# Kernel optimization log

Measured on AMD Instinct MI355X. Metric: run time of the kernel, lower is better.

Reference implementation:

```python
import jax, jax.numpy as jnp
import numpy as np

B, S, D = 4, 2048, 1024
NEG = -1e10

def setup_inputs() -> dict:
    key = jax.random.key(0)
    ks = jax.random.split(key, 10)
    inv = 1.0 / np.sqrt(D)
    return {
        "Q": jax.random.normal(ks[0], (B, S, D), dtype=jnp.float32),
        "K": jax.random.normal(ks[1], (B, S, D), dtype=jnp.float32),
        "V": jax.random.normal(ks[2], (B, S, D), dtype=jnp.float32),
        "attention_mask": jax.random.randint(ks[3], (B, 1, S), 0, 2, dtype=jnp.int32),
        "Wq": jax.random.uniform(ks[4], (D, D), jnp.float32, -inv, inv),
        "bq": jnp.zeros((D,), jnp.float32),
        "Wk": jax.random.uniform(ks[5], (D, D), jnp.float32, -inv, inv),
        "bk": jnp.zeros((D,), jnp.float32),
        "Wv": jax.random.uniform(ks[6], (D, D), jnp.float32, -inv, inv),
        "bv": jnp.zeros((D,), jnp.float32),
    }

def reference(Q, K, V, attention_mask, Wq, bq, Wk, bk, Wv, bv):
    # QKV projections (dropout is identity in eval mode)
    q = jnp.einsum('bsd,ed->bse', Q, Wq) + bq  # [B,S,D]
    k = jnp.einsum('bsd,ed->bse', K, Wk) + bk
    v = jnp.einsum('bsd,ed->bse', V, Wv) + bv
    scores = jnp.einsum('bqd,bkd->bqk', q, k) / jnp.sqrt(jnp.float32(D))  # [B,S,S]
    scores = jnp.where(attention_mask == 0, jnp.float32(NEG), scores)
    # additive causal mask: upper triangle (diag=1) gets NEG
    causal = jnp.triu(jnp.full((S, S), NEG, dtype=jnp.float32), k=1)
    scores = scores + causal
    attn = jax.nn.softmax(scores, axis=-1)
    return jnp.einsum('bqk,bkd->bqd', attn, v)
```

## Files before the change

kernel.cpp:

```cpp
#include <hip/hip_runtime.h>
#include <hip/hip_bf16.h>

typedef __bf16 bf16x8 __attribute__((ext_vector_type(8)));
typedef float floatx4 __attribute__((ext_vector_type(4)));
typedef unsigned short ushort_t;

__device__ __forceinline__ bf16x8 load8f(const float* p) {
  const float4* q = reinterpret_cast<const float4*>(p);
  float4 x = q[0], y = q[1];
  bf16x8 r;
  r[0] = (__bf16)x.x; r[1] = (__bf16)x.y; r[2] = (__bf16)x.z; r[3] = (__bf16)x.w;
  r[4] = (__bf16)y.x; r[5] = (__bf16)y.y; r[6] = (__bf16)y.z; r[7] = (__bf16)y.w;
  return r;
}

__device__ __forceinline__ void storeC(float* C, long idx, float v) { C[idx] = v; }
__device__ __forceinline__ void storeC(ushort_t* C, long idx, float v) {
  __bf16 b = (__bf16)v;
  C[idx] = __builtin_bit_cast(ushort_t, b);
}

__device__ __forceinline__ void glds16(const ushort_t* g, ushort_t* l) {
  __builtin_amdgcn_global_load_lds(
      (const __attribute__((address_space(1))) void*)g,
      (__attribute__((address_space(3))) void*)l, 16, 0, 0);
}

__device__ __forceinline__ void bar_raw()  { asm volatile("s_barrier" ::: "memory"); }
__device__ __forceinline__ void wait_vm0() { asm volatile("s_waitcnt vmcnt(0)" ::: "memory"); }
__device__ __forceinline__ void wlg12() {
  asm volatile("s_waitcnt lgkmcnt(12)" ::: "memory");
  __builtin_amdgcn_sched_barrier(0);
}
__device__ __forceinline__ void wlg8() {
  asm volatile("s_waitcnt lgkmcnt(8)" ::: "memory");
  __builtin_amdgcn_sched_barrier(0);
}
__device__ __forceinline__ void wlg0() {
  asm volatile("s_waitcnt lgkmcnt(0)" ::: "memory");
  __builtin_amdgcn_sched_barrier(0);
}

__global__ __launch_bounds__(256) void cvt3m(
    const float* __restrict__ Q, const float* __restrict__ K,
    const float* __restrict__ V, const float* __restrict__ Wq,
    const float* __restrict__ Wk, const float* __restrict__ Wv,
    ushort_t* __restrict__ dstQ, ushort_t* __restrict__ dstW,
    long nq, long nw,
    const int* __restrict__ mask, int* __restrict__ j0, int S, int B)
{
  const int z = blockIdx.y;
  const long bq = nq >> 11;
  long x = blockIdx.x;
  const float* s; ushort_t* d; long n;
  if (x < bq) {
    s = (z == 0) ? Q : ((z == 1) ? K : V);
    d = dstQ + (long)z * nq; n = nq;
  } else {
    x -= bq;
    s = (z == 0) ? Wq : ((z == 1) ? Wk : Wv);
    d = dstW + (long)z * nw; n = nw;
  }
  const long i = ((x * 256) + threadIdx.x) * 8;
  if (i < n) {
    bf16x8 v = load8f(s + i);
    *reinterpret_cast<bf16x8*>(d + i) = v;
  }
  if (z == 0 && (int)blockIdx.x < B) {
    const int b = blockIdx.x;
    const int* m = mask + (long)b * S;
    const int tid = threadIdx.x;
    int best = S;
    for (int j = tid; j < S; j += 256)
      if (m[j] != 0) best = min(best, j);
    #pragma unroll
    for (int off = 32; off; off >>= 1)
      best = min(best, __shfl_xor(best, off));
    __shared__ int red[4];
    if ((tid & 63) == 0) red[tid >> 6] = best;
    __syncthreads();
    if (tid == 0) j0[b] = min(min(red[0], red[1]), min(red[2], red[3]));
  }
}

template<typename TC>
__device__ __forceinline__ void gemm256_core(
    const ushort_t* __restrict__ Apan,
    const ushort_t* __restrict__ Bpan,
    const float* __restrict__ bias, int bias_mode,
    TC* __restrict__ C, int bm, int bn, int N, int K, int G, float alpha)
{
  __shared__ ushort_t Ab[2][2][128 * 64];
  __shared__ ushort_t Bb[2][2][128 * 64];

  const int tid = threadIdx.x;
  const int wv = tid >> 6;
  const int lane = tid & 63;
  const int wr = wv >> 2, wc = wv & 3;
  const int lr = lane & 15, lq = lane >> 4;

  const int q0 = tid << 4;
  const int r0 = q0 >> 7;
  const int c0 = ((q0 & 127) ^ ((r0 & 7) << 4)) >> 1;
  const int lo0 = q0 >> 1;
  const int lo1 = lo0 + 4096;
  const long Kl = K;

  const ushort_t* As0 = Apan + (long)r0 * Kl + c0;
  const ushort_t* Bs0 = Bpan + (long)r0 * Kl + c0;

  auto stA = [&](int t, int h) {
    const ushort_t* s = As0 + (long)(h * 128) * Kl + t * 64;
    ushort_t* d = &Ab[t & 1][h][0];
    glds16(s, d + lo0);
    glds16(s + 64 * Kl, d + lo1);
  };
  auto stB = [&](int t, int h) {
    const ushort_t* s = Bs0 + (long)(h * 128) * Kl + t * 64;
    ushort_t* d = &Bb[t & 1][h][0];
    glds16(s, d + lo0);
    glds16(s + 64 * Kl, d + lo1);
  };

  const int aco0 = ((lq * 16) ^ ((lr & 7) << 4)) >> 1;
  const int aco1 = ((64 + lq * 16) ^ ((lr & 7) << 4)) >> 1;

  floatx4 acc[8][4];
  #pragma unroll
  for (int i = 0; i < 8; ++i)
    #pragma unroll
    for (int j = 0; j < 4; ++j)
      acc[i][j] = (floatx4){0.f, 0.f, 0.f, 0.f};

  bf16x8 a0[4][2], a1[4][2], b0[2][2], b1[2][2];

  auto ldA4 = [&](bf16x8 (&a)[4][2], int buf, int i0) {
    const ushort_t* Ah = &Ab[buf][wr][lr * 64];
    #pragma unroll
    for (int i = 0; i < 4; ++i) {
      a[i][0] = *reinterpret_cast<const bf16x8*>(Ah + (i0 + i) * 1024 + aco0);
      a[i][1] = *reinterpret_cast<const bf16x8*>(Ah + (i0 + i) * 1024 + aco1);
    }
  };
  auto ldB2 = [&](bf16x8 (&b)[2][2], int buf, int j0) {
    const ushort_t* Bh = &Bb[buf][wc >> 1][(wc & 1) * 4096 + lr * 64];
    #pragma unroll
    for (int j = 0; j < 2; ++j) {
      b[j][0] = *reinterpret_cast<const bf16x8*>(Bh + (j0 + j) * 1024 + aco0);
      b[j][1] = *reinterpret_cast<const bf16x8*>(Bh + (j0 + j) * 1024 + aco1);
    }
  };
  auto MM = [&](int I0, bf16x8 (&AF)[4][2], int J0, bf16x8 (&BF)[2][2]) {
    #pragma unroll
    for (int i = 0; i < 4; ++i)
      #pragma unroll
      for (int j = 0; j < 2; ++j) {
        acc[I0 + i][J0 + j] = __builtin_amdgcn_mfma_f32_16x16x32_bf16(
            AF[i][0], BF[j][0], acc[I0 + i][J0 + j], 0, 0, 0);
        acc[I0 + i][J0 + j] = __builtin_amdgcn_mfma_f32_16x16x32_bf16(
            AF[i][1], BF[j][1], acc[I0 + i][J0 + j], 0, 0, 0);
      }
  };

  stA(0, 0); stA(0, 1); stB(0, 0); stB(0, 1);
  wait_vm0();
  bar_raw();

  for (int t = 0; t < G; ++t) {
    const int buf = t & 1;
    if (t + 1 < G) { stA(t + 1, 0); stA(t + 1, 1); stB(t + 1, 0); stB(t + 1, 1); }
    __builtin_amdgcn_sched_barrier(0);
    ldA4(a0, buf, 0);
    ldB2(b0, buf, 0);
    __builtin_amdgcn_sched_barrier(0);
    ldB2(b1, buf, 2);
    __builtin_amdgcn_sched_barrier(0);
    ldA4(a1, buf, 4);
    __builtin_amdgcn_sched_barrier(0);
    wlg12();
    __builtin_amdgcn_s_setprio(1);
    MM(0, a0, 0, b0);
    __builtin_amdgcn_s_setprio(0);
    wlg8();
    __builtin_amdgcn_s_setprio(1);
    MM(0, a0, 2, b1);
    __builtin_amdgcn_s_setprio(0);
    wlg0();
    __builtin_amdgcn_s_setprio(1);
    MM(4, a1, 0, b0);
    MM(4, a1, 2, b1);
    __builtin_amdgcn_s_setprio(0);
    wait_vm0();
    bar_raw();
  }

  #pragma unroll
  for (int i = 0; i < 8; ++i) {
    #pragma unroll
    for (int j = 0; j < 4; ++j) {
      const int row0 = bm * 256 + wr * 128 + i * 16 + lq * 4;
      const int col  = bn * 256 + wc * 64 + j * 16 + lr;
      #pragma unroll
      for (int r = 0; r < 4; ++r) {
        float v = acc[i][j][r] * alpha;
        if (bias_mode == 1) v += bias[col];
        else if (bias_mode == 2) v += bias[row0 + r];
        storeC(C, (long)(row0 + r) * N + col, v);
      }
    }
  }
}

__global__ __launch_bounds__(512) void proj8(
    const ushort_t* __restrict__ Qb, const ushort_t* __restrict__ Wqb,
    const float* __restrict__ bq, const float* __restrict__ bk,
    const float* __restrict__ bv,
    ushort_t* __restrict__ qk, ushort_t* __restrict__ vT,
    long NQ, long NW)
{
  const int h = blockIdx.x;
  const int s = (h & 7) * 48 + (h >> 3);
  int bm, bn, N, mode;
  const ushort_t *A, *Bp;
  ushort_t* Cc;
  const float* bias;
  if (s < 256) {
    const int z = s >> 7, r = s & 127;
    bm = r >> 2; bn = r & 3;
    A  = Qb + (long)z * NQ + (long)bm * 256 * 1024;
    Bp = Wqb + (long)z * NW + (long)bn * 256 * 1024;
    Cc = qk + (long)z * NQ;
    bias = z ? bk : bq; mode = 1; N = 1024;
  } else {
    const int u = s - 256, vb = u >> 5, r = u & 31;
    bm = r >> 3; bn = r & 7;
    A  = Wqb + 2 * NW + (long)bm * 256 * 1024;
    Bp = Qb + 2 * NQ + (long)vb * (2048L * 1024) + (long)bn * 256 * 1024;
    Cc = vT + (long)vb * (1024L * 2048);
    bias = bv; mode = 2; N = 2048;
  }
  gemm256_core<ushort_t>(A, Bp, bias, mode, Cc, bm, bn, N, 1024, 16, 1.0f);
}

__global__ __launch_bounds__(512) void scores8(
    const ushort_t* __restrict__ qb, const ushort_t* __restrict__ kb,
    ushort_t* __restrict__ Sc, const int* __restrict__ j0p)
{
  const int h = blockIdx.x;
  const int job = (h & 7) * 32 + (h >> 3);
  const int bz = job >> 6;
  const int s = job & 63;
  int bm, bn;
  if (s < 36) {
    int r = 0;
    while ((r + 1) * (r + 2) / 2 <= s) ++r;
    bm = r; bn = s - r * (r + 1) / 2;
  } else {
    int u = s - 36, r = 0;
    while (u >= 7 - r) { u -= 7 - r; ++r; }
    bm = r; bn = r + 1 + u;
  }
  if (bn > bm && j0p[bz] <= bm * 256) return;
  const long SD = 2048L * 1024;
  gemm256_core<ushort_t>(qb + (long)bz * SD + (long)bm * 256 * 1024,
                         kb + (long)bz * SD + (long)bn * 256 * 1024,
                         nullptr, 0, Sc + (long)bz * 2048 * 2048,
                         bm, bn, 2048, 1024, 16, 0.03125f);
}

__global__ __launch_bounds__(512) void pv8(
    const ushort_t* __restrict__ P, const ushort_t* __restrict__ vT,
    float* __restrict__ out, float* __restrict__ scr,
    const int* __restrict__ j0p)
{
  const int h = blockIdx.x;
  const int job = (h & 7) * 32 + (h >> 3);
  const int bz = job >> 6;
  const int r = job & 63;
  const int bm = r >> 3;
  const int kh = (r >> 2) & 1;
  const int bn = r & 3;

  const int Gf = (j0p[bz] <= bm * 256) ? (bm + 1) * 4 : 32;
  int g0, g1;
  if (Gf > 8) {
    const int half = Gf >> 1;
    g0 = kh ? half : 0;
    g1 = kh ? Gf : half;
  } else {
    if (kh) return;
    g0 = 0; g1 = Gf;
  }

  float* Cc = kh ? (scr + (long)bz * (2048L * 1024))
                 : (out + (long)bz * (2048L * 1024));
  gemm256_core<float>(
      P  + (long)bz * (2048L * 2048) + (long)bm * 256 * 2048 + g0 * 64,
      vT + (long)bz * (1024L * 2048) + (long)bn * 256 * 2048 + g0 * 64,
      nullptr, 0, Cc, bm, bn, 1024, 2048, g1 - g0, 1.0f);
}

__global__ __launch_bounds__(256) void pv_combine(
    float* __restrict__ out, const float* __restrict__ scr,
    const int* __restrict__ j0p)
{
  const long u = (((long)blockIdx.x * 256) + threadIdx.x) * 8;
  const int bz = (int)(u >> 21);
  const long rem = u & ((1L << 21) - 1);
  const int row = (int)(rem >> 10);
  const int bm = row >> 8;
  const int Gf = (j0p[bz] <= bm * 256) ? (bm + 1) * 4 : 32;
  if (Gf <= 8) return;
  float4* o = reinterpret_cast<float4*>(out + u);
  const float4* s = reinterpret_cast<const float4*>(scr + u);
  float4 o0 = o[0], o1 = o[1], s0 = s[0], s1 = s[1];
  o0.x += s0.x; o0.y += s0.y; o0.z += s0.z; o0.w += s0.w;
  o1.x += s1.x; o1.y += s1.y; o1.z += s1.z; o1.w += s1.w;
  o[0] = o0; o[1] = o1;
}

__global__ __launch_bounds__(256) void softmax_causal(
    const ushort_t* __restrict__ Sc, ushort_t* __restrict__ P,
    const int* __restrict__ mask, const int* __restrict__ j0p, int S)
{
  const int i = blockIdx.x, b = blockIdx.y;
  const ushort_t* row = Sc + ((long)b * S + i) * S;
  ushort_t* prow = P + ((long)b * S + i) * S;
  const int* mrow = mask + (long)b * S;
  const int tid = threadIdx.x;
  const int lane = tid & 63, wave = tid >> 6;
  const int j0 = tid * 8;
  __shared__ float red[4];

  const int blk = i >> 8;
  const int jmax = (j0p[b] <= (blk << 8)) ? ((blk + 1) << 8) : S;
  const bool act = (j0 < jmax);

  float vals[8];
  float mymax = -3.4e38f;
  if (act) {
    bf16x8 sv = *reinterpret_cast<const bf16x8*>(row + j0);
    const int4* mp = reinterpret_cast<const int4*>(mrow + j0);
    int4 m0 = mp[0], m1 = mp[1];
    int mk[8] = {m0.x, m0.y, m0.z, m0.w, m1.x, m1.y, m1.z, m1.w};
    #pragma unroll
    for (int u = 0; u < 8; ++u) {
      const int j = j0 + u;
      float v = (float)sv[u];
      if (mk[u] == 0) v = -1e10f;
      if (j > i) v += -1e10f;
      vals[u] = v;
      mymax = fmaxf(mymax, v);
    }
  }
  #pragma unroll
  for (int off = 32; off; off >>= 1)
    mymax = fmaxf(mymax, __shfl_xor(mymax, off));
  if (lane == 0) red[wave] = mymax;
  __syncthreads();
  const float m = fmaxf(fmaxf(red[0], red[1]), fmaxf(red[2], red[3]));
  __syncthreads();

  float sum = 0.f;
  if (act) {
    #pragma unroll
    for (int u = 0; u < 8; ++u) {
      const float e = __expf(vals[u] - m);
      vals[u] = e;
      sum += e;
    }
  }
  #pragma unroll
  for (int off = 32; off; off >>= 1)
    sum += __shfl_xor(sum, off);
  if (lane == 0) red[wave] = sum;
  __syncthreads();
  const float tot = red[0] + red[1] + red[2] + red[3];
  const float inv = 1.0f / tot;

  if (act) {
    bf16x8 pv;
    #pragma unroll
    for (int u = 0; u < 8; ++u) pv[u] = (__bf16)(vals[u] * inv);
    *reinterpret_cast<bf16x8*>(prow + j0) = pv;
  }
}

extern "C" void kernel_launch(void* const* d_in, const int* in_sizes, int n_in,
                              void* d_out, int out_size, void* d_ws, size_t ws_size,
                              hipStream_t stream)
{
  const int B = 4, S = 2048, D = 1024;
  const float* Q  = (const float*)d_in[0];
  const float* K  = (const float*)d_in[1];
  const float* V  = (const float*)d_in[2];
  const int*   am = (const int*)d_in[3];
  const float* Wq = (const float*)d_in[4];
  const float* bq = (const float*)d_in[5];
  const float* Wk = (const float*)d_in[6];
  const float* bk = (const float*)d_in[7];
  const float* Wv = (const float*)d_in[8];
  const float* bv = (const float*)d_in[9];
  float* out = (float*)d_out;

  const long MS = (long)B * S;
  const long NQ = MS * D;
  const long NW = (long)D * D;

  ushort_t* qb = (ushort_t*)d_ws;
  ushort_t* kb = qb + NQ;
  ushort_t* vT = kb + NQ;
  ushort_t* Qb = vT + NQ;
  ushort_t* Wqb = Qb + 3 * NQ;
  int* j0 = (int*)(Wqb + 3 * NW);
  ushort_t* Sc = Qb;
  ushort_t* P  = qb;
  float* scr   = (float*)Qb;

  cvt3m<<<dim3((int)(NQ / 2048 + NW / 2048), 3), dim3(256), 0, stream>>>(
      Q, K, V, Wq, Wk, Wv, Qb, Wqb, NQ, NW, am, j0, S, B);

  proj8<<<dim3(384), dim3(512), 0, stream>>>(Qb, Wqb, bq, bk, bv, qb, vT, NQ, NW);

  scores8<<<dim3(256), dim3(512), 0, stream>>>(qb, kb, Sc, j0);

  softmax_causal<<<dim3(S, B), dim3(256), 0, stream>>>(Sc, P, am, j0, S);

  pv8<<<dim3(256), dim3(512), 0, stream>>>(P, vT, out, scr, j0);
  pv_combine<<<dim3((int)(MS * D / 8 / 256)), dim3(256), 0, stream>>>(out, scr, j0);
}
```

Baseline: 325.3 us.

## Fuse fp32-to-bf16 activation conversion into projection GEMM loads

The separate pre-pass that converted the Q, K and V activations from fp32 to bf16 is removed. The projection GEMM now loads fp32 activation tiles into registers, packs them to bf16 and writes them to swizzled LDS, interleaved with the MFMA pipeline, while the weights keep the async global-to-LDS path. This removes a full read and write of the activation tensors through HBM. In exchange each GEMM reads twice as many bytes for activations and spends extra VGPRs and VALU work on conversion, which may cut latency hiding.

```diff
diff --git a/kernel.cpp b/kernel.cpp
--- a/kernel.cpp
+++ b/kernel.cpp
@@ -13,6 +13,12 @@
   r[4] = (__bf16)y.x; r[5] = (__bf16)y.y; r[6] = (__bf16)y.z; r[7] = (__bf16)y.w;
   return r;
 }
+__device__ __forceinline__ bf16x8 pack8(float4 x, float4 y) {
+  bf16x8 r;
+  r[0] = (__bf16)x.x; r[1] = (__bf16)x.y; r[2] = (__bf16)x.z; r[3] = (__bf16)x.w;
+  r[4] = (__bf16)y.x; r[5] = (__bf16)y.y; r[6] = (__bf16)y.z; r[7] = (__bf16)y.w;
+  return r;
+}
 
 __device__ __forceinline__ void storeC(float* C, long idx, float v) { C[idx] = v; }
 __device__ __forceinline__ void storeC(ushort_t* C, long idx, float v) {
@@ -28,6 +34,14 @@
 
 __device__ __forceinline__ void bar_raw()  { asm volatile("s_barrier" ::: "memory"); }
 __device__ __forceinline__ void wait_vm0() { asm volatile("s_waitcnt vmcnt(0)" ::: "memory"); }
+__device__ __forceinline__ void wv4s() {
+  asm volatile("s_waitcnt vmcnt(4)" ::: "memory");
+  __builtin_amdgcn_sched_barrier(0);
+}
+__device__ __forceinline__ void wv0s() {
+  asm volatile("s_waitcnt vmcnt(0)" ::: "memory");
+  __builtin_amdgcn_sched_barrier(0);
+}
 __device__ __forceinline__ void wlg12() {
   asm volatile("s_waitcnt lgkmcnt(12)" ::: "memory");
   __builtin_amdgcn_sched_barrier(0);
@@ -36,33 +50,25 @@
   asm volatile("s_waitcnt lgkmcnt(8)" ::: "memory");
   __builtin_amdgcn_sched_barrier(0);
 }
+__device__ __forceinline__ void wlg4() {
+  asm volatile("s_waitcnt lgkmcnt(4)" ::: "memory");
+  __builtin_amdgcn_sched_barrier(0);
+}
 __device__ __forceinline__ void wlg0() {
   asm volatile("s_waitcnt lgkmcnt(0)" ::: "memory");
   __builtin_amdgcn_sched_barrier(0);
 }
 
 __global__ __launch_bounds__(256) void cvt3m(
-    const float* __restrict__ Q, const float* __restrict__ K,
-    const float* __restrict__ V, const float* __restrict__ Wq,
-    const float* __restrict__ Wk, const float* __restrict__ Wv,
-    ushort_t* __restrict__ dstQ, ushort_t* __restrict__ dstW,
-    long nq, long nw,
+    const float* __restrict__ Wq, const float* __restrict__ Wk,
+    const float* __restrict__ Wv, ushort_t* __restrict__ dstW, long nw,
     const int* __restrict__ mask, int* __restrict__ j0, int S, int B)
 {
   const int z = blockIdx.y;
-  const long bq = nq >> 11;
-  long x = blockIdx.x;
-  const float* s; ushort_t* d; long n;
-  if (x < bq) {
-    s = (z == 0) ? Q : ((z == 1) ? K : V);
-    d = dstQ + (long)z * nq; n = nq;
-  } else {
-    x -= bq;
-    s = (z == 0) ? Wq : ((z == 1) ? Wk : Wv);
-    d = dstW + (long)z * nw; n = nw;
-  }
-  const long i = ((x * 256) + threadIdx.x) * 8;
-  if (i < n) {
+  const float* s = (z == 0) ? Wq : ((z == 1) ? Wk : Wv);
+  ushort_t* d = dstW + (long)z * nw;
+  const long i = (((long)blockIdx.x * 256) + threadIdx.x) * 8;
+  if (i < nw) {
     bf16x8 v = load8f(s + i);
     *reinterpret_cast<bf16x8*>(d + i) = v;
   }
@@ -85,8 +91,7 @@
 
 template<typename TC>
 __device__ __forceinline__ void gemm256_core(
-    const ushort_t* __restrict__ Apan,
-    const ushort_t* __restrict__ Bpan,
+    const ushort_t* __restrict__ Apan, const ushort_t* __restrict__ Bpan,
     const float* __restrict__ bias, int bias_mode,
     TC* __restrict__ C, int bm, int bn, int N, int K, int G, float alpha)
 {
@@ -211,35 +216,206 @@
   }
 }
 
-__global__ __launch_bounds__(512) void proj8(
-    const ushort_t* __restrict__ Qb, const ushort_t* __restrict__ Wqb,
+template<typename TC, bool F32A>
+__device__ __forceinline__ void gemm256f(
+    ushort_t* __restrict__ AbL, ushort_t* __restrict__ BbL,
+    const float* __restrict__ Fsrc, const ushort_t* __restrict__ Hsrc,
+    const float* __restrict__ bias, int bias_mode,
+    TC* __restrict__ C, int bm, int bn, int N, float alpha)
+{
+  const int K = 1024, G = 16;
+
+  const int tid = threadIdx.x;
+  const int wv = tid >> 6;
+  const int lane = tid & 63;
+  const int wr = wv >> 2, wc = wv & 3;
+  const int lr = lane & 15, lq = lane >> 4;
+
+  auto AB = [&](int buf, int h) -> ushort_t* { return AbL + ((buf * 2 + h) << 13); };
+  auto BB = [&](int buf, int h) -> ushort_t* { return BbL + ((buf * 2 + h) << 13); };
+
+  const int q0 = tid << 4;
+  const int r0 = q0 >> 7;
+  const int c0 = ((q0 & 127) ^ ((r0 & 7) << 4)) >> 1;
+  const int lo0 = q0 >> 1;
+  const int lo1 = lo0 + 4096;
+  const ushort_t* Hs0 = Hsrc + (long)r0 * K + c0;
+  auto stH = [&](int t) {
+    #pragma unroll
+    for (int h = 0; h < 2; ++h) {
+      const ushort_t* s = Hs0 + (long)(h * 128) * K + t * 64;
+      ushort_t* d = F32A ? BB(t & 1, h) : AB(t & 1, h);
+      glds16(s, d + lo0);
+      glds16(s + 64 * K, d + lo1);
+    }
+  };
+
+  const int rr = tid >> 1, cc = (tid & 1) << 5;
+  const int rl = rr & 127, hh = rr >> 7;
+  const int sw = (rl & 7) << 3;
+  const float* Fs0 = Fsrc + (long)rr * K + cc;
+  float4 fl0[4], fl1[4];
+  auto ldF0 = [&](int t) {
+    const float4* p = reinterpret_cast<const float4*>(Fs0 + t * 64);
+    #pragma unroll
+    for (int i = 0; i < 4; ++i) fl0[i] = p[i];
+  };
+  auto ldF1 = [&](int t) {
+    const float4* p = reinterpret_cast<const float4*>(Fs0 + t * 64 + 16);
+    #pragma unroll
+    for (int i = 0; i < 4; ++i) fl1[i] = p[i];
+  };
+  auto wrF0 = [&](int t) {
+    ushort_t* dst = (F32A ? AB(t & 1, hh) : BB(t & 1, hh)) + rl * 64;
+    *reinterpret_cast<bf16x8*>(dst + ((cc + 0) ^ sw)) = pack8(fl0[0], fl0[1]);
+    *reinterpret_cast<bf16x8*>(dst + ((cc + 8) ^ sw)) = pack8(fl0[2], fl0[3]);
+  };
+  auto wrF1 = [&](int t) {
+    ushort_t* dst = (F32A ? AB(t & 1, hh) : BB(t & 1, hh)) + rl * 64;
+    *reinterpret_cast<bf16x8*>(dst + ((cc + 16) ^ sw)) = pack8(fl1[0], fl1[1]);
+    *reinterpret_cast<bf16x8*>(dst + ((cc + 24) ^ sw)) = pack8(fl1[2], fl1[3]);
+  };
+
+  const int aco0 = ((lq * 16) ^ ((lr & 7) << 4)) >> 1;
+  const int aco1 = ((64 + lq * 16) ^ ((lr & 7) << 4)) >> 1;
+
+  floatx4 acc[8][4];
+  #pragma unroll
+  for (int i = 0; i < 8; ++i)
+    #pragma unroll
+    for (int j = 0; j < 4; ++j)
+      acc[i][j] = (floatx4){0.f, 0.f, 0.f, 0.f};
+
+  bf16x8 a0[4][2], a1[4][2], b0[2][2], b1[2][2];
+
+  auto ldA4 = [&](bf16x8 (&a)[4][2], int buf, int i0) {
+    const ushort_t* Ah = AB(buf, wr) + lr * 64;
+    #pragma unroll
+    for (int i = 0; i < 4; ++i) {
+      a[i][0] = *reinterpret_cast<const bf16x8*>(Ah + (i0 + i) * 1024 + aco0);
+      a[i][1] = *reinterpret_cast<const bf16x8*>(Ah + (i0 + i) * 1024 + aco1);
+    }
+  };
+  auto ldB2 = [&](bf16x8 (&b)[2][2], int buf, int j0) {
+    const ushort_t* Bh = BB(buf, wc >> 1) + (wc & 1) * 4096 + lr * 64;
+    #pragma unroll
+    for (int j = 0; j < 2; ++j) {
+      b[j][0] = *reinterpret_cast<const bf16x8*>(Bh + (j0 + j) * 1024 + aco0);
+      b[j][1] = *reinterpret_cast<const bf16x8*>(Bh + (j0 + j) * 1024 + aco1);
+    }
+  };
+  auto MM = [&](int I0, bf16x8 (&AF)[4][2], int J0, bf16x8 (&BF)[2][2]) {
+    #pragma unroll
+    for (int i = 0; i < 4; ++i)
+      #pragma unroll
+      for (int j = 0; j < 2; ++j) {
+        acc[I0 + i][J0 + j] = __builtin_amdgcn_mfma_f32_16x16x32_bf16(
+            AF[i][0], BF[j][0], acc[I0 + i][J0 + j], 0, 0, 0);
+        acc[I0 + i][J0 + j] = __builtin_amdgcn_mfma_f32_16x16x32_bf16(
+            AF[i][1], BF[j][1], acc[I0 + i][J0 + j], 0, 0, 0);
+      }
+  };
+
+  ldF0(0); stH(0);
+  wv4s();
+  wrF0(0);
+  ldF1(0);
+  wv0s();
+  wrF1(0);
+  wlg0();
+  bar_raw();
+
+  for (int t = 0; t < G; ++t) {
+    const int buf = t & 1;
+    const bool pre = (t + 1 < G);
+    if (pre) {
+      ldF0(t + 1);
+      stH(t + 1);
+    }
+    __builtin_amdgcn_sched_barrier(0);
+    ldA4(a0, buf, 0);
+    ldB2(b0, buf, 0);
+    __builtin_amdgcn_sched_barrier(0);
+    ldB2(b1, buf, 2);
+    __builtin_amdgcn_sched_barrier(0);
+    wlg4();
+    __builtin_amdgcn_s_setprio(1);
+    MM(0, a0, 0, b0);
+    __builtin_amdgcn_s_setprio(0);
+    wlg0();
+    __builtin_amdgcn_s_setprio(1);
+    MM(0, a0, 2, b1);
+    __builtin_amdgcn_s_setprio(0);
+    if (pre) {
+      wv4s();
+      wrF0(t + 1);
+      ldF1(t + 1);
+      __builtin_amdgcn_sched_barrier(0);
+    }
+    ldA4(a1, buf, 4);
+    __builtin_amdgcn_sched_barrier(0);
+    wlg0();
+    __builtin_amdgcn_s_setprio(1);
+    MM(4, a1, 0, b0);
+    MM(4, a1, 2, b1);
+    __builtin_amdgcn_s_setprio(0);
+    if (pre) {
+      wv0s();
+      wrF1(t + 1);
+      wlg0();
+    } else {
+      wait_vm0();
+    }
+    bar_raw();
+  }
+
+  #pragma unroll
+  for (int i = 0; i < 8; ++i) {
+    #pragma unroll
+    for (int j = 0; j < 4; ++j) {
+      const int row0 = bm * 256 + wr * 128 + i * 16 + lq * 4;
+      const int col  = bn * 256 + wc * 64 + j * 16 + lr;
+      #pragma unroll
+      for (int r = 0; r < 4; ++r) {
+        float v = acc[i][j][r] * alpha;
+        if (bias_mode == 1) v += bias[col];
+        else if (bias_mode == 2) v += bias[row0 + r];
+        storeC(C, (long)(row0 + r) * N + col, v);
+      }
+    }
+  }
+}
+
+__global__ __launch_bounds__(512) void projF(
+    const float* __restrict__ Qf, const float* __restrict__ Kf,
+    const float* __restrict__ Vf, const ushort_t* __restrict__ Wb,
     const float* __restrict__ bq, const float* __restrict__ bk,
     const float* __restrict__ bv,
     ushort_t* __restrict__ qk, ushort_t* __restrict__ vT,
     long NQ, long NW)
 {
+  __shared__ ushort_t AbS[2][2][128 * 64];
+  __shared__ ushort_t BbS[2][2][128 * 64];
+  ushort_t* AbL = &AbS[0][0][0];
+  ushort_t* BbL = &BbS[0][0][0];
+
   const int h = blockIdx.x;
   const int s = (h & 7) * 48 + (h >> 3);
-  int bm, bn, N, mode;
-  const ushort_t *A, *Bp;
-  ushort_t* Cc;
-  const float* bias;
   if (s < 256) {
     const int z = s >> 7, r = s & 127;
-    bm = r >> 2; bn = r & 3;
-    A  = Qb + (long)z * NQ + (long)bm * 256 * 1024;
-    Bp = Wqb + (long)z * NW + (long)bn * 256 * 1024;
-    Cc = qk + (long)z * NQ;
-    bias = z ? bk : bq; mode = 1; N = 1024;
+    const int bm = r >> 2, bn = r & 3;
+    const float* F = (z ? Kf : Qf) + (long)bm * 256 * 1024;
+    const ushort_t* H = Wb + (long)z * NW + (long)bn * 256 * 1024;
+    gemm256f<ushort_t, true>(AbL, BbL, F, H, z ? bk : bq, 1,
+                             qk + (long)z * NQ, bm, bn, 1024, 1.0f);
   } else {
     const int u = s - 256, vb = u >> 5, r = u & 31;
-    bm = r >> 3; bn = r & 7;
-    A  = Wqb + 2 * NW + (long)bm * 256 * 1024;
-    Bp = Qb + 2 * NQ + (long)vb * (2048L * 1024) + (long)bn * 256 * 1024;
-    Cc = vT + (long)vb * (1024L * 2048);
-    bias = bv; mode = 2; N = 2048;
-  }
-  gemm256_core<ushort_t>(A, Bp, bias, mode, Cc, bm, bn, N, 1024, 16, 1.0f);
+    const int bm = r >> 3, bn = r & 7;
+    const float* F = Vf + (long)vb * (2048L * 1024) + (long)bn * 256 * 1024;
+    const ushort_t* H = Wb + 2 * NW + (long)bm * 256 * 1024;
+    gemm256f<ushort_t, false>(AbL, BbL, F, H, bv, 2,
+                              vT + (long)vb * (1024L * 2048), bm, bn, 2048, 1.0f);
+  }
 }
 
 __global__ __launch_bounds__(512) void scores8(
@@ -410,17 +586,18 @@
   ushort_t* qb = (ushort_t*)d_ws;
   ushort_t* kb = qb + NQ;
   ushort_t* vT = kb + NQ;
-  ushort_t* Qb = vT + NQ;
-  ushort_t* Wqb = Qb + 3 * NQ;
+  ushort_t* ScB = vT + NQ;
+  ushort_t* Wqb = ScB + 3 * NQ;
   int* j0 = (int*)(Wqb + 3 * NW);
-  ushort_t* Sc = Qb;
+  ushort_t* Sc = ScB;
   ushort_t* P  = qb;
-  float* scr   = (float*)Qb;
-
-  cvt3m<<<dim3((int)(NQ / 2048 + NW / 2048), 3), dim3(256), 0, stream>>>(
-      Q, K, V, Wq, Wk, Wv, Qb, Wqb, NQ, NW, am, j0, S, B);
-
-  proj8<<<dim3(384), dim3(512), 0, stream>>>(Qb, Wqb, bq, bk, bv, qb, vT, NQ, NW);
+  float* scr   = (float*)ScB;
+
+  cvt3m<<<dim3((int)(NW / 2048), 3), dim3(256), 0, stream>>>(
+      Wq, Wk, Wv, Wqb, NW, am, j0, S, B);
+
+  projF<<<dim3(384), dim3(512), 0, stream>>>(Q, K, V, Wqb, bq, bk, bv,
+                                             qb, vT, NQ, NW);
 
   scores8<<<dim3(256), dim3(512), 0, stream>>>(qb, kb, Sc, j0);
 
```

Result: slower. 360.1 us (+10.7%).
